# Optimization experiments

Hardware: AMD Instinct MI355X
Metric: run time of the kernel (lower is better)

The kernel has to match this reference:

```python
import jax, jax.numpy as jnp
import numpy as np
from jax import lax


def setup_inputs() -> dict:
    key = jax.random.key(0)
    k1, k2 = jax.random.split(key)
    B, H, T, F, R = 8, 16, 4096, 64, 65
    a = jax.random.normal(k1, (B, H, T, R), dtype=jnp.float32)
    v = jax.random.normal(k2, (B, H, T, F), dtype=jnp.float32)
    return {"a": a, "v": v}


def _unfold_matmul(a, v):
    # out[b,h,t,f] = sum_r a[b,h,t,r] * v[b,h, t + r - R//2, f]  (zero-padded in time)
    B, H, T, F = v.shape
    R = a.shape[-1]
    pad = R // 2
    vp = jnp.pad(v, ((0, 0), (0, 0), (pad, pad), (0, 0)))  # (B,H,T+R-1,F)

    def body(acc, r):
        vs = lax.dynamic_slice_in_dim(vp, r, T, axis=2)      # shifted values (B,H,T,F)
        ar = lax.dynamic_slice_in_dim(a, r, 1, axis=3)       # (B,H,T,1)
        return acc + ar * vs, None

    out, _ = lax.scan(body, jnp.zeros_like(v), jnp.arange(R))
    return out


def reference(a, v):
    return _unfold_matmul(a, v)
```

## Files before the change

kernel.cpp:

```cpp
#include <hip/hip_runtime.h>


#define TT 4096
#define RRR 65
#define FF 64
#define SA_S 100

typedef short bf16x8 __attribute__((ext_vector_type(8)));
typedef float f32x16 __attribute__((ext_vector_type(16)));

__device__ __forceinline__ unsigned short f2bf(float x) {
    unsigned int u = __float_as_uint(x);
    u += 0x7fff + ((u >> 16) & 1);
    return (unsigned short)(u >> 16);
}
__device__ __forceinline__ unsigned pk2(float lo, float hi) {
    return (unsigned)f2bf(lo) | ((unsigned)f2bf(hi) << 16);
}

#define BAR() do {                                                             \
    asm volatile("s_waitcnt lgkmcnt(0)" ::: "memory");                         \
    __builtin_amdgcn_sched_barrier(0);                                         \
    __builtin_amdgcn_s_barrier();                                              \
    __builtin_amdgcn_sched_barrier(0);                                         \
} while (0)

__global__ __launch_bounds__(256, 8)
void unfold_mfma(const float* __restrict__ a, const float* __restrict__ v,
                 float* __restrict__ out) {
    __shared__ __align__(16) unsigned short sa[64 * SA_S];

    const int tid = threadIdx.x;
    const int f   = tid & 63;
    const int wv  = tid >> 6;
    const int n   = f & 31;
    const int hi  = f >> 5;
    const int wr  = wv >> 1;
    const int wc  = wv & 1;
    const int Rw  = 32 * wr + n;

    const int lid = ((blockIdx.x & 7) << 10) | (blockIdx.x >> 3);
    const int bh = lid >> 6;
    const int t0 = (lid & 63) << 6;

    const float* arow = a + ((size_t)bh * TT + t0) * RRR;
    const float* vsl  = v + (size_t)bh * TT * FF;

    float4 aq[4];
    #pragma unroll
    for (int it = 0; it < 4; ++it) {
        int lin = tid + it * 256;
        if (lin < 64 * 15) {
            int R = lin / 15, j = lin - R * 15;
            int r0 = (4 - (R & 3)) & 3;
            aq[it] = *(const float4*)(arow + (size_t)R * RRR + r0 + 4 * j);
        }
    }
    float ae[2];
    #pragma unroll
    for (int it = 0; it < 2; ++it) {
        int lin = tid + it * 256;
        if (lin < 64 * 5) {
            int R = lin / 5, e = lin - R * 5;
            int r0 = (4 - (R & 3)) & 3;
            int r = (e < r0) ? e : 60 + e;
            ae[it] = arow[(size_t)R * RRR + r];
        }
    }

    {
        uint4 z = make_uint4(0, 0, 0, 0);
        uint4* sp = (uint4*)sa;
        #pragma unroll
        for (int it = 0; it < 4; ++it) {
            int lin = tid + it * 256;
            if (lin < (64 * SA_S) / 8) sp[lin] = z;
        }
    }
    BAR();

    #pragma unroll
    for (int it = 0; it < 4; ++it) {
        int lin = tid + it * 256;
        if (lin < 64 * 15) {
            int R = lin / 15, j = lin - R * 15;
            int r0 = (4 - (R & 3)) & 3;
            int rq = r0 + 4 * j;
            float4 q = aq[it];
            uint2 pw; pw.x = pk2(q.x, q.y); pw.y = pk2(q.z, q.w);
            *(uint2*)&sa[R * SA_S + (R & 31) + rq] = pw;
        }
    }
    #pragma unroll
    for (int it = 0; it < 2; ++it) {
        int lin = tid + it * 256;
        if (lin < 64 * 5) {
            int R = lin / 5, e = lin - R * 5;
            int r0 = (4 - (R & 3)) & 3;
            int r = (e < r0) ? e : 60 + e;
            sa[R * SA_S + (R & 31) + r] = f2bf(ae[it]);
        }
    }
    BAR();

    const int fcol = 32 * wc + n;
    const int tb   = t0 + 32 * wr - 32 + 8 * hi;
    const float* vp = vsl + fcol;

    f32x16 acc = {};
    if (t0 >= 32 && t0 + 96 <= TT) {
        #pragma unroll
        for (int kb = 0; kb < 6; ++kb) {
            float x[8];
            #pragma unroll
            for (int j = 0; j < 8; ++j)
                x[j] = vp[(size_t)(tb + 16 * kb + j) * FF];
            union { bf16x8 v8; unsigned u[4]; } bu;
            bu.u[0] = pk2(x[0], x[1]); bu.u[1] = pk2(x[2], x[3]);
            bu.u[2] = pk2(x[4], x[5]); bu.u[3] = pk2(x[6], x[7]);
            bf16x8 af = *(const bf16x8*)&sa[Rw * SA_S + kb * 16 + hi * 8];
            acc = __builtin_amdgcn_mfma_f32_32x32x16_bf16(af, bu.v8, acc, 0, 0, 0);
        }
    } else {
        #pragma unroll
        for (int kb = 0; kb < 6; ++kb) {
            float x[8];
            #pragma unroll
            for (int j = 0; j < 8; ++j) {
                int t = tb + 16 * kb + j;
                x[j] = (t >= 0 && t < TT) ? vp[(size_t)t * FF] : 0.f;
            }
            union { bf16x8 v8; unsigned u[4]; } bu;
            bu.u[0] = pk2(x[0], x[1]); bu.u[1] = pk2(x[2], x[3]);
            bu.u[2] = pk2(x[4], x[5]); bu.u[3] = pk2(x[6], x[7]);
            bf16x8 af = *(const bf16x8*)&sa[Rw * SA_S + kb * 16 + hi * 8];
            acc = __builtin_amdgcn_mfma_f32_32x32x16_bf16(af, bu.v8, acc, 0, 0, 0);
        }
    }

    float* op = out + (size_t)bh * TT * FF + (size_t)(t0 + 32 * wr) * FF + 32 * wc;
    #pragma unroll
    for (int reg = 0; reg < 16; ++reg) {
        int row = (reg & 3) + 8 * (reg >> 2) + 4 * hi;
        __builtin_nontemporal_store(acc[reg], &op[row * FF + n]);
    }
}

extern "C" void kernel_launch(void* const* d_in, const int* in_sizes, int n_in,
                              void* d_out, int out_size, void* d_ws, size_t ws_size,
                              hipStream_t stream) {
    const float* a = (const float*)d_in[0];
    const float* v = (const float*)d_in[1];
    float* out = (float*)d_out;

    const int BH = in_sizes[1] / (TT * FF);
    const int grid = BH * 64;

    unfold_mfma<<<grid, 256, 0, stream>>>(a, v, out);
}
```

Baseline: 69.74 us.

## Load banded A operand directly from global into registers, dropping LDS staging

Removes the shared-memory staging of the banded 'a' matrix, along with its zero-fill and two barriers. Each lane now loads its 8 A values per k-block straight from global memory, masks out entries outside the band, and converts them to bf16 before the MFMA. Occupancy hint lowered from 8 to 4 blocks per SU to allow more registers. The trade-off is more scattered, uncoalesced global loads for 'a', some of which are redundant or masked, in exchange for no LDS traffic or synchronisation.

```diff
diff --git a/kernel.cpp b/kernel.cpp
--- a/kernel.cpp
+++ b/kernel.cpp
@@ -4,7 +4,6 @@
 #define TT 4096
 #define RRR 65
 #define FF 64
-#define SA_S 100
 
 typedef short bf16x8 __attribute__((ext_vector_type(8)));
 typedef float f32x16 __attribute__((ext_vector_type(16)));
@@ -18,18 +17,9 @@
     return (unsigned)f2bf(lo) | ((unsigned)f2bf(hi) << 16);
 }
 
-#define BAR() do {                                                             \
-    asm volatile("s_waitcnt lgkmcnt(0)" ::: "memory");                         \
-    __builtin_amdgcn_sched_barrier(0);                                         \
-    __builtin_amdgcn_s_barrier();                                              \
-    __builtin_amdgcn_sched_barrier(0);                                         \
-} while (0)
-
-__global__ __launch_bounds__(256, 8)
+__global__ __launch_bounds__(256, 4)
 void unfold_mfma(const float* __restrict__ a, const float* __restrict__ v,
                  float* __restrict__ out) {
-    __shared__ __align__(16) unsigned short sa[64 * SA_S];
-
     const int tid = threadIdx.x;
     const int f   = tid & 63;
     const int wv  = tid >> 6;
@@ -43,99 +33,40 @@
     const int bh = lid >> 6;
     const int t0 = (lid & 63) << 6;
 
-    const float* arow = a + ((size_t)bh * TT + t0) * RRR;
-    const float* vsl  = v + (size_t)bh * TT * FF;
-
-    float4 aq[4];
-    #pragma unroll
-    for (int it = 0; it < 4; ++it) {
-        int lin = tid + it * 256;
-        if (lin < 64 * 15) {
-            int R = lin / 15, j = lin - R * 15;
-            int r0 = (4 - (R & 3)) & 3;
-            aq[it] = *(const float4*)(arow + (size_t)R * RRR + r0 + 4 * j);
-        }
-    }
-    float ae[2];
-    #pragma unroll
-    for (int it = 0; it < 2; ++it) {
-        int lin = tid + it * 256;
-        if (lin < 64 * 5) {
-            int R = lin / 5, e = lin - R * 5;
-            int r0 = (4 - (R & 3)) & 3;
-            int r = (e < r0) ? e : 60 + e;
-            ae[it] = arow[(size_t)R * RRR + r];
-        }
-    }
-
-    {
-        uint4 z = make_uint4(0, 0, 0, 0);
-        uint4* sp = (uint4*)sa;
-        #pragma unroll
-        for (int it = 0; it < 4; ++it) {
-            int lin = tid + it * 256;
-            if (lin < (64 * SA_S) / 8) sp[lin] = z;
-        }
-    }
-    BAR();
-
-    #pragma unroll
-    for (int it = 0; it < 4; ++it) {
-        int lin = tid + it * 256;
-        if (lin < 64 * 15) {
-            int R = lin / 15, j = lin - R * 15;
-            int r0 = (4 - (R & 3)) & 3;
-            int rq = r0 + 4 * j;
-            float4 q = aq[it];
-            uint2 pw; pw.x = pk2(q.x, q.y); pw.y = pk2(q.z, q.w);
-            *(uint2*)&sa[R * SA_S + (R & 31) + rq] = pw;
-        }
-    }
-    #pragma unroll
-    for (int it = 0; it < 2; ++it) {
-        int lin = tid + it * 256;
-        if (lin < 64 * 5) {
-            int R = lin / 5, e = lin - R * 5;
-            int r0 = (4 - (R & 3)) & 3;
-            int r = (e < r0) ? e : 60 + e;
-            sa[R * SA_S + (R & 31) + r] = f2bf(ae[it]);
-        }
-    }
-    BAR();
-
-    const int fcol = 32 * wc + n;
-    const int tb   = t0 + 32 * wr - 32 + 8 * hi;
-    const float* vp = vsl + fcol;
+    const float* arow = a + (size_t)(bh * TT + t0 + Rw) * RRR - n;
+    const float* vp   = v + (size_t)bh * TT * FF + 32 * wc + n;
+    const int    tb   = t0 + 32 * wr - 32 + 8 * hi;
+    const bool interior = (t0 >= 32) && (t0 + 96 <= TT);
 
     f32x16 acc = {};
-    if (t0 >= 32 && t0 + 96 <= TT) {
+    #pragma unroll
+    for (int kb = 0; kb < 6; ++kb) {
+        const int cp = kb * 16 + hi * 8;
+        float av[8], xv[8];
         #pragma unroll
-        for (int kb = 0; kb < 6; ++kb) {
-            float x[8];
+        for (int j = 0; j < 8; ++j)
+            av[j] = arow[cp + j];
+        if (interior) {
             #pragma unroll
             for (int j = 0; j < 8; ++j)
-                x[j] = vp[(size_t)(tb + 16 * kb + j) * FF];
-            union { bf16x8 v8; unsigned u[4]; } bu;
-            bu.u[0] = pk2(x[0], x[1]); bu.u[1] = pk2(x[2], x[3]);
-            bu.u[2] = pk2(x[4], x[5]); bu.u[3] = pk2(x[6], x[7]);
-            bf16x8 af = *(const bf16x8*)&sa[Rw * SA_S + kb * 16 + hi * 8];
-            acc = __builtin_amdgcn_mfma_f32_32x32x16_bf16(af, bu.v8, acc, 0, 0, 0);
-        }
-    } else {
-        #pragma unroll
-        for (int kb = 0; kb < 6; ++kb) {
-            float x[8];
+                xv[j] = vp[(size_t)(tb + 16 * kb + j) * FF];
+        } else {
             #pragma unroll
             for (int j = 0; j < 8; ++j) {
                 int t = tb + 16 * kb + j;
-                x[j] = (t >= 0 && t < TT) ? vp[(size_t)t * FF] : 0.f;
+                xv[j] = (t >= 0 && t < TT) ? vp[(size_t)t * FF] : 0.f;
             }
-            union { bf16x8 v8; unsigned u[4]; } bu;
-            bu.u[0] = pk2(x[0], x[1]); bu.u[1] = pk2(x[2], x[3]);
-            bu.u[2] = pk2(x[4], x[5]); bu.u[3] = pk2(x[6], x[7]);
-            bf16x8 af = *(const bf16x8*)&sa[Rw * SA_S + kb * 16 + hi * 8];
-            acc = __builtin_amdgcn_mfma_f32_32x32x16_bf16(af, bu.v8, acc, 0, 0, 0);
         }
+        #pragma unroll
+        for (int j = 0; j < 8; ++j)
+            av[j] = ((unsigned)(cp + j - n) <= 64u) ? av[j] : 0.f;
+
+        union { bf16x8 v8; unsigned u[4]; } au, bu;
+        au.u[0] = pk2(av[0], av[1]); au.u[1] = pk2(av[2], av[3]);
+        au.u[2] = pk2(av[4], av[5]); au.u[3] = pk2(av[6], av[7]);
+        bu.u[0] = pk2(xv[0], xv[1]); bu.u[1] = pk2(xv[2], xv[3]);
+        bu.u[2] = pk2(xv[4], xv[5]); bu.u[3] = pk2(xv[6], xv[7]);
+        acc = __builtin_amdgcn_mfma_f32_32x32x16_bf16(au.v8, bu.v8, acc, 0, 0, 0);
     }
 
     float* op = out + (size_t)bh * TT * FF + (size_t)(t0 + 32 * wr) * FF + 32 * wc;
```

New measurement: 86.43 us. 23.9% more time.
